# Kernel optimization log

Measured on AMD Instinct MI355X. Metric: run time of the kernel, lower is better.

## Reference

```python
import jax, jax.numpy as jnp
import numpy as np

B, N, DIM = 1, 1024, 384
H, DK, DV = 8, 16, 16
PD = 128  # pairwise_repr_dim
SCALAR_SCALE = (3 * DK) ** -0.5
PAIR_SCALE = 3.0 ** -0.5


def setup_inputs() -> dict:
    key = jax.random.key(0)
    ks = jax.random.split(key, 9)
    return {
        "single_repr": jax.random.normal(ks[0], (B, N, DIM), jnp.float32),
        "pairwise_repr": jax.random.normal(ks[1], (B, N, N, PD), jnp.float32),
        "rotations": jax.random.normal(ks[2], (B, N, 3, 3), jnp.float32),
        "translations": jax.random.normal(ks[3], (B, N, 3), jnp.float32),
        "mask": jnp.ones((B, N), dtype=bool),
        "Wq": jax.random.normal(ks[4], (DIM, H * DK), jnp.float32) * 0.02,
        "Wk": jax.random.normal(ks[5], (DIM, H * DK), jnp.float32) * 0.02,
        "Wv": jax.random.normal(ks[6], (DIM, H * DV), jnp.float32) * 0.02,
        "Wb": jax.random.normal(ks[7], (PD, H), jnp.float32) * 0.02,
        "bb": jnp.zeros((H,), jnp.float32),
    }


def _split_heads(t, d):
    # [b, n, h*d] -> [b, h, n, d]
    b, n, _ = t.shape
    return t.reshape(b, n, H, d).transpose(0, 2, 1, 3)


def reference(single_repr, pairwise_repr, rotations, translations, mask, Wq, Wk, Wv, Wb, bb):
    x = single_repr
    b, n, _ = x.shape
    q = _split_heads(x @ Wq, DK)  # [b, h, n, dk]
    k = _split_heads(x @ Wk, DK)
    v = _split_heads(x @ Wv, DV)

    # scalar QK logits + learned pairwise additive bias
    logits = jnp.einsum('bhid,bhjd->bhij', q, k) * SCALAR_SCALE
    bias = (jnp.einsum('bijd,dh->bijh', pairwise_repr, Wb) + bb) * PAIR_SCALE
    logits = logits + bias.transpose(0, 3, 1, 2)  # [b, h, i, j]

    mask2d = mask[:, None, :, None] & mask[:, None, None, :]  # [b, 1, i, j]
    neg = -jnp.finfo(logits.dtype).max
    logits = jnp.where(mask2d, logits, neg)

    attn = jax.nn.softmax(logits, axis=-1)

    # dual aggregation: attn @ V and attn-weighted pairwise reduction
    res_scalar = jnp.einsum('bhij,bhjd->bhid', attn, v)            # [b, h, n, dv]
    res_pair = jnp.einsum('bhij,bijd->bhid', attn, pairwise_repr)   # [b, h, n, pd]

    res_scalar = res_scalar.transpose(0, 2, 1, 3).reshape(b, n, H * DV)
    res_pair = res_pair.transpose(0, 2, 1, 3).reshape(b, n, H * PD)
    return jnp.concatenate([res_scalar, res_pair], axis=-1)  # [b, n, h*(dv+pd)]
```

## Files before the change

### kernel.cpp

```cpp
#include <hip/hip_runtime.h>

#define N 1024
#define DIM 384
#define H 8
#define DK 16
#define DV 16
#define PD 128
#define HD 128
#define TJ 32
#define NTILES (N / TJ)
#define PSTR 132
#define OUTW 1152

#define SCALAR_SCALE 0.14433756729740643f
#define PAIR_SCALE   0.5773502691896258f

__global__ __launch_bounds__(256) void qkv_kernel(
    const float* __restrict__ x,
    const float* __restrict__ Wq, const float* __restrict__ Wk,
    const float* __restrict__ Wv,
    float* __restrict__ qkv)
{
    const int mat = blockIdx.x % 3;
    const int rt  = blockIdx.x / 3;
    const float* __restrict__ W = (mat == 0) ? Wq : (mat == 1) ? Wk : Wv;
    float* __restrict__ out = qkv + (size_t)mat * N * HD;

    __shared__ float xs[64][33];
    __shared__ float ws[32][128];

    const int t  = threadIdx.x;
    const int tc = (t & 31) * 4;
    const int tr = (t >> 5) * 8;

    float acc[8][4];
#pragma unroll
    for (int r = 0; r < 8; r++) {
        acc[r][0] = 0.f; acc[r][1] = 0.f; acc[r][2] = 0.f; acc[r][3] = 0.f;
    }

    for (int kk = 0; kk < DIM; kk += 32) {
#pragma unroll
        for (int u = 0; u < 8; u++) {
            int idx = t + u * 256;
            int r = idx >> 5, c = idx & 31;
            xs[r][c] = x[(size_t)(rt * 64 + r) * DIM + kk + c];
        }
#pragma unroll
        for (int u = 0; u < 4; u++) {
            int idx = t + u * 256;
            int r = idx >> 5, c4 = (idx & 31) * 4;
            *(float4*)&ws[r][c4] = *(const float4*)&W[(size_t)(kk + r) * HD + c4];
        }
        __syncthreads();
#pragma unroll
        for (int kkk = 0; kkk < 32; kkk++) {
            float4 b = *(float4*)&ws[kkk][tc];
#pragma unroll
            for (int r = 0; r < 8; r++) {
                float a = xs[tr + r][kkk];
                acc[r][0] += a * b.x; acc[r][1] += a * b.y;
                acc[r][2] += a * b.z; acc[r][3] += a * b.w;
            }
        }
        __syncthreads();
    }
#pragma unroll
    for (int r = 0; r < 8; r++) {
        *(float4*)&out[(size_t)(rt * 64 + tr + r) * HD + tc] =
            make_float4(acc[r][0], acc[r][1], acc[r][2], acc[r][3]);
    }
}

__global__ __launch_bounds__(256) void attn_kernel(
    const float* __restrict__ pair,
    const float* __restrict__ Wb,
    const float* __restrict__ bbp,
    const float* __restrict__ qkv,
    float* __restrict__ out)
{
    const int i = blockIdx.x;
    const int t = threadIdx.x;
    const float* __restrict__ q = qkv;
    const float* __restrict__ k = qkv + (size_t)N * HD;
    const float* __restrict__ v = qkv + (size_t)2 * N * HD;

    __shared__ float pt[TJ][PSTR];
    __shared__ float wbt[H][PSTR];
    __shared__ float ps[TJ][8];
    __shared__ float red[256][4];
    __shared__ float lred[H];

    {
        float4 w4 = *(const float4*)&Wb[t * 4];
        int i0 = t * 4;
        wbt[(i0 + 0) & 7][(i0 + 0) >> 3] = w4.x;
        wbt[(i0 + 1) & 7][(i0 + 1) >> 3] = w4.y;
        wbt[(i0 + 2) & 7][(i0 + 2) >> 3] = w4.z;
        wbt[(i0 + 3) & 7][(i0 + 3) >> 3] = w4.w;
    }

    const int jB = t >> 3, hB = t & 7;
    const int s2 = t & 31, jg = t >> 5;
    const int hv = s2 >> 2;

    const float4 q0 = *(const float4*)&q[(size_t)i * HD + hB * 16 + 0];
    const float4 q1 = *(const float4*)&q[(size_t)i * HD + hB * 16 + 4];
    const float4 q2 = *(const float4*)&q[(size_t)i * HD + hB * 16 + 8];
    const float4 q3 = *(const float4*)&q[(size_t)i * HD + hB * 16 + 12];
    const float bbh = bbp[hB];

    float accp[8][4];
#pragma unroll
    for (int h = 0; h < 8; h++) {
        accp[h][0] = 0.f; accp[h][1] = 0.f; accp[h][2] = 0.f; accp[h][3] = 0.f;
    }
    float accv[4] = {0.f, 0.f, 0.f, 0.f};
    float lpart = 0.f;

    for (int tile = 0; tile < NTILES; tile++) {
        const int j0 = tile * TJ;
        __syncthreads();
#pragma unroll
        for (int u = 0; u < 4; u++) {
            int idx = t + u * 256;
            int r = idx >> 5, c4 = (idx & 31) * 4;
            *(float4*)&pt[r][c4] =
                *(const float4*)&pair[((size_t)i * N + (j0 + r)) * PD + c4];
        }
        __syncthreads();

        float a0 = 0.f, a1 = 0.f, a2 = 0.f, a3 = 0.f;
#pragma unroll
        for (int s = 0; s < 32; s++) {
            float4 pv = *(float4*)&pt[jB][s * 4];
            float4 wv = *(float4*)&wbt[hB][s * 4];
            a0 += pv.x * wv.x; a1 += pv.y * wv.y;
            a2 += pv.z * wv.z; a3 += pv.w * wv.w;
        }
        float accb = (a0 + a1) + (a2 + a3);

        const float* kr = &k[(size_t)(j0 + jB) * HD + hB * 16];
        float4 k0 = *(const float4*)&kr[0];
        float4 k1 = *(const float4*)&kr[4];
        float4 k2 = *(const float4*)&kr[8];
        float4 k3 = *(const float4*)&kr[12];
        float d0 = q0.x * k0.x + q0.y * k0.y + q0.z * k0.z + q0.w * k0.w;
        float d1 = q1.x * k1.x + q1.y * k1.y + q1.z * k1.z + q1.w * k1.w;
        float d2 = q2.x * k2.x + q2.y * k2.y + q2.z * k2.z + q2.w * k2.w;
        float d3 = q3.x * k3.x + q3.y * k3.y + q3.z * k3.z + q3.w * k3.w;
        float accqk = (d0 + d1) + (d2 + d3);

        float logit = accqk * SCALAR_SCALE + (accb + bbh) * PAIR_SCALE;
        float p = __expf(logit);
        ps[jB][hB] = p;
        lpart += p;
        __syncthreads();

#pragma unroll
        for (int jo = 0; jo < 4; jo++) {
            int j = jg * 4 + jo;
            float4 pr  = *(float4*)&pt[j][s2 * 4];
            float4 p03 = *(float4*)&ps[j][0];
            float4 p47 = *(float4*)&ps[j][4];
            accp[0][0] += p03.x * pr.x; accp[0][1] += p03.x * pr.y;
            accp[0][2] += p03.x * pr.z; accp[0][3] += p03.x * pr.w;
            accp[1][0] += p03.y * pr.x; accp[1][1] += p03.y * pr.y;
            accp[1][2] += p03.y * pr.z; accp[1][3] += p03.y * pr.w;
            accp[2][0] += p03.z * pr.x; accp[2][1] += p03.z * pr.y;
            accp[2][2] += p03.z * pr.z; accp[2][3] += p03.z * pr.w;
            accp[3][0] += p03.w * pr.x; accp[3][1] += p03.w * pr.y;
            accp[3][2] += p03.w * pr.z; accp[3][3] += p03.w * pr.w;
            accp[4][0] += p47.x * pr.x; accp[4][1] += p47.x * pr.y;
            accp[4][2] += p47.x * pr.z; accp[4][3] += p47.x * pr.w;
            accp[5][0] += p47.y * pr.x; accp[5][1] += p47.y * pr.y;
            accp[5][2] += p47.y * pr.z; accp[5][3] += p47.y * pr.w;
            accp[6][0] += p47.z * pr.x; accp[6][1] += p47.z * pr.y;
            accp[6][2] += p47.z * pr.z; accp[6][3] += p47.z * pr.w;
            accp[7][0] += p47.w * pr.x; accp[7][1] += p47.w * pr.y;
            accp[7][2] += p47.w * pr.z; accp[7][3] += p47.w * pr.w;

            float pvv = ps[j][hv];
            float4 vv = *(const float4*)&v[(size_t)(j0 + j) * HD + s2 * 4];
            accv[0] += pvv * vv.x; accv[1] += pvv * vv.y;
            accv[2] += pvv * vv.z; accv[3] += pvv * vv.w;
        }
    }

    __syncthreads();
    red[t][0] = lpart;
    __syncthreads();
    if (t < H) {
        float s = 0.f;
#pragma unroll
        for (int jj = 0; jj < 32; jj++) s += red[t + 8 * jj][0];
        lred[t] = 1.f / s;
    }
    __syncthreads();

    red[t][0] = accv[0]; red[t][1] = accv[1]; red[t][2] = accv[2]; red[t][3] = accv[3];
    __syncthreads();
    if (t < 32) {
        float o0 = 0.f, o1 = 0.f, o2 = 0.f, o3 = 0.f;
#pragma unroll
        for (int g = 0; g < 8; g++) {
            o0 += red[g * 32 + t][0]; o1 += red[g * 32 + t][1];
            o2 += red[g * 32 + t][2]; o3 += red[g * 32 + t][3];
        }
        float li = lred[t >> 2];
        *(float4*)&out[(size_t)i * OUTW + t * 4] =
            make_float4(o0 * li, o1 * li, o2 * li, o3 * li);
    }

    for (int h = 0; h < 8; h++) {
        __syncthreads();
        red[t][0] = accp[h][0]; red[t][1] = accp[h][1];
        red[t][2] = accp[h][2]; red[t][3] = accp[h][3];
        __syncthreads();
        if (t < 32) {
            float o0 = 0.f, o1 = 0.f, o2 = 0.f, o3 = 0.f;
#pragma unroll
            for (int g = 0; g < 8; g++) {
                o0 += red[g * 32 + t][0]; o1 += red[g * 32 + t][1];
                o2 += red[g * 32 + t][2]; o3 += red[g * 32 + t][3];
            }
            float li = lred[h];
            *(float4*)&out[(size_t)i * OUTW + 128 + h * 128 + t * 4] =
                make_float4(o0 * li, o1 * li, o2 * li, o3 * li);
        }
    }
}

extern "C" void kernel_launch(void* const* d_in, const int* in_sizes, int n_in,
                              void* d_out, int out_size, void* d_ws, size_t ws_size,
                              hipStream_t stream) {
    const float* x    = (const float*)d_in[0];
    const float* pair = (const float*)d_in[1];
    const float* Wq   = (const float*)d_in[5];
    const float* Wk   = (const float*)d_in[6];
    const float* Wv   = (const float*)d_in[7];
    const float* Wb   = (const float*)d_in[8];
    const float* bb   = (const float*)d_in[9];
    float* out = (float*)d_out;
    float* qkv = (float*)d_ws;

    qkv_kernel<<<48, 256, 0, stream>>>(x, Wq, Wk, Wv, qkv);
    attn_kernel<<<N, 256, 0, stream>>>(pair, Wb, bb, qkv, out);
}
```

Measured before the change: 777.8 us.

## Double-buffer pairwise tiles with async global-to-LDS loads and XOR swizzle

Replaces the synchronous register-staged load of each pairwise tile with global_load_lds direct-to-LDS copies into a double buffer, prefetching the next tile while the current one is computed. The padded layout is replaced by an XOR-swizzled column layout to avoid bank conflicts, and the reduction scratch is unioned with the bias weights to cut LDS so four blocks can run per CU. The hand-written waitcnt/barrier sequence adds ordering risk around the async loads, and vmcnt(0) at the top of each tile may limit how much overlap is achieved.

```diff
diff --git a/kernel.cpp b/kernel.cpp
--- a/kernel.cpp
+++ b/kernel.cpp
@@ -9,7 +9,6 @@
 #define HD 128
 #define TJ 32
 #define NTILES (N / TJ)
-#define PSTR 132
 #define OUTW 1152
 
 #define SCALAR_SCALE 0.14433756729740643f
@@ -72,7 +71,7 @@
     }
 }
 
-__global__ __launch_bounds__(256) void attn_kernel(
+__global__ __launch_bounds__(256, 4) void attn_kernel(
     const float* __restrict__ pair,
     const float* __restrict__ Wb,
     const float* __restrict__ bbp,
@@ -81,15 +80,21 @@
 {
     const int i = blockIdx.x;
     const int t = threadIdx.x;
+    const int l  = t & 63;
+    const int wid = t >> 6;
     const float* __restrict__ q = qkv;
     const float* __restrict__ k = qkv + (size_t)N * HD;
     const float* __restrict__ v = qkv + (size_t)2 * N * HD;
 
-    __shared__ float pt[TJ][PSTR];
-    __shared__ float wbt[H][PSTR];
-    __shared__ float ps[TJ][8];
-    __shared__ float red[256][4];
+    __shared__ float pt[2][TJ][PD];
+    __shared__ union __align__(16) SU {
+        struct { float wbt[H][132]; float ps[TJ][H]; } bp;
+        float red[256][4];
+    } su;
     __shared__ float lred[H];
+
+    float (*wbt)[132] = su.bp.wbt;
+    float (*ps)[H]    = su.bp.ps;
 
     {
         float4 w4 = *(const float4*)&Wb[t * 4];
@@ -118,33 +123,51 @@
     float accv[4] = {0.f, 0.f, 0.f, 0.f};
     float lpart = 0.f;
 
+    auto stage = [&](int buf, int jbase) {
+#pragma unroll
+        for (int u = 0; u < 4; u++) {
+            int idx = u * 256 + wid * 64 + l;
+            int r = idx >> 5;
+            int g = (idx & 31) ^ (r & 7);
+            const float* src = &pair[((size_t)i * N + (size_t)(jbase + r)) * PD + g * 4];
+            float* dst = &pt[buf][0][0] + (size_t)(u * 256 + wid * 64) * 4;
+            __builtin_amdgcn_global_load_lds(
+                (const __attribute__((address_space(1))) void*)src,
+                (__attribute__((address_space(3))) void*)dst, 16, 0, 0);
+        }
+    };
+
+    stage(0, 0);
+
     for (int tile = 0; tile < NTILES; tile++) {
-        const int j0 = tile * TJ;
-        __syncthreads();
-#pragma unroll
-        for (int u = 0; u < 4; u++) {
-            int idx = t + u * 256;
-            int r = idx >> 5, c4 = (idx & 31) * 4;
-            *(float4*)&pt[r][c4] =
-                *(const float4*)&pair[((size_t)i * N + (j0 + r)) * PD + c4];
-        }
-        __syncthreads();
-
-        float a0 = 0.f, a1 = 0.f, a2 = 0.f, a3 = 0.f;
-#pragma unroll
-        for (int s = 0; s < 32; s++) {
-            float4 pv = *(float4*)&pt[jB][s * 4];
-            float4 wv = *(float4*)&wbt[hB][s * 4];
-            a0 += pv.x * wv.x; a1 += pv.y * wv.y;
-            a2 += pv.z * wv.z; a3 += pv.w * wv.w;
-        }
-        float accb = (a0 + a1) + (a2 + a3);
+        const int j0  = tile * TJ;
+        const int buf = tile & 1;
+
+        asm volatile("s_waitcnt vmcnt(0) lgkmcnt(0)" ::: "memory");
+        __builtin_amdgcn_s_barrier();
+        asm volatile("" ::: "memory");
 
         const float* kr = &k[(size_t)(j0 + jB) * HD + hB * 16];
         float4 k0 = *(const float4*)&kr[0];
         float4 k1 = *(const float4*)&kr[4];
         float4 k2 = *(const float4*)&kr[8];
         float4 k3 = *(const float4*)&kr[12];
+        __builtin_amdgcn_sched_barrier(0);
+
+        if (tile + 1 < NTILES) stage(buf ^ 1, j0 + TJ);
+
+        const float* ptr = &pt[buf][jB][0];
+        const int cswz = jB & 7;
+        float a0 = 0.f, a1 = 0.f, a2 = 0.f, a3 = 0.f;
+#pragma unroll
+        for (int s = 0; s < 32; s++) {
+            float4 pv  = *(const float4*)&ptr[((s ^ cswz) * 4)];
+            float4 wv4 = *(const float4*)&wbt[hB][s * 4];
+            a0 += pv.x * wv4.x; a1 += pv.y * wv4.y;
+            a2 += pv.z * wv4.z; a3 += pv.w * wv4.w;
+        }
+        float accb = (a0 + a1) + (a2 + a3);
+
         float d0 = q0.x * k0.x + q0.y * k0.y + q0.z * k0.z + q0.w * k0.w;
         float d1 = q1.x * k1.x + q1.y * k1.y + q1.z * k1.z + q1.w * k1.w;
         float d2 = q2.x * k2.x + q2.y * k2.y + q2.z * k2.z + q2.w * k2.w;
@@ -155,14 +178,17 @@
         float p = __expf(logit);
         ps[jB][hB] = p;
         lpart += p;
-        __syncthreads();
+
+        asm volatile("s_waitcnt lgkmcnt(0)" ::: "memory");
+        __builtin_amdgcn_s_barrier();
+        asm volatile("" ::: "memory");
 
 #pragma unroll
         for (int jo = 0; jo < 4; jo++) {
             int j = jg * 4 + jo;
-            float4 pr  = *(float4*)&pt[j][s2 * 4];
-            float4 p03 = *(float4*)&ps[j][0];
-            float4 p47 = *(float4*)&ps[j][4];
+            float4 pr  = *(const float4*)&pt[buf][j][((s2 ^ (j & 7)) * 4)];
+            float4 p03 = *(const float4*)&ps[j][0];
+            float4 p47 = *(const float4*)&ps[j][4];
             accp[0][0] += p03.x * pr.x; accp[0][1] += p03.x * pr.y;
             accp[0][2] += p03.x * pr.z; accp[0][3] += p03.x * pr.w;
             accp[1][0] += p03.y * pr.x; accp[1][1] += p03.y * pr.y;
@@ -187,6 +213,8 @@
         }
     }
 
+    float (*red)[4] = su.red;
+
     __syncthreads();
     red[t][0] = lpart;
     __syncthreads();
```

After: 912.8 us. 17.4% more time.
